# Optimization experiments

Hardware: AMD Instinct MI355X
Metric: run time of the kernel (lower is better)

## Reference

```python
import jax, jax.numpy as jnp
import numpy as np

DEPTH = 17                 # levels of the complete binary tree
N = 2**DEPTH - 1           # 131071 nodes, BFS order: children of n are 2n+1, 2n+2
IN_DIM = 128
HID = 128
OUT = 128


def setup_inputs() -> dict:
    key = jax.random.key(0)
    ks = jax.random.split(key, 20)

    def lin_w(k, o, i):
        s = 1.0 / np.sqrt(i)
        return jax.random.uniform(k, (o, i), minval=-s, maxval=s, dtype=jnp.float32)

    def lin_b(k, o, i):
        s = 1.0 / np.sqrt(i)
        return jax.random.uniform(k, (o,), minval=-s, maxval=s, dtype=jnp.float32)

    inp = {"x": jax.random.normal(ks[0], (N, IN_DIM), dtype=jnp.float32)}
    # complete binary tree, parent -> child edges (row0=src/parent, row1=dst/child)
    child = np.arange(1, N)
    parent = (child - 1) // 2
    inp["edge_index"] = jnp.asarray(np.stack([parent, child]), dtype=jnp.int32)
    names = [("Wi", "bWi", IN_DIM), ("Ui", "bUi", HID),
             ("Wf", "bWf", IN_DIM), ("Uf", "bUf", HID),
             ("Wo", "bWo", IN_DIM), ("Uo", "bUo", HID),
             ("Wu", "bWu", IN_DIM), ("Uu", "bUu", HID)]
    ki = 1
    for wname, bname, idim in names:
        inp[wname] = lin_w(ks[ki], HID, idim)
        inp[bname] = lin_b(ks[ki + 1], HID, idim)
        ki += 2
    inp["Wp"] = lin_w(ks[17], OUT, HID)
    inp["bWp"] = lin_b(ks[18], OUT, HID)
    return inp


def reference(x, edge_index, Wi, bWi, Ui, bUi, Wf, bWf, Uf, bUf,
              Wo, bWo, Uo, bUo, Wu, bWu, Uu, bUu, Wp, bWp):
    # edge_index encodes the complete binary tree in BFS order (children of n
    # are 2n+1 and 2n+2), so the recursion batches exactly by tree level.
    # Precompute input-side gate projections for ALL nodes in 4 GEMMs
    # (equivalent to calling W_*(x[node]) per node in the torch recursion).
    xi = x @ Wi.T + bWi            # (N, H)
    xf = x @ Wf.T + bWf
    xo = x @ Wo.T + bWo
    xu = x @ Wu.T + bWu

    h_next = None  # hidden states of the level below (children)
    c_next = None
    for d in range(DEPTH - 1, -1, -1):   # bottom-up over tree levels
        s = 2**d - 1                     # first node index of level d
        cnt = 2**d                       # nodes at level d
        li, lf, lo, lu = xi[s:s + cnt], xf[s:s + cnt], xo[s:s + cnt], xu[s:s + cnt]
        if h_next is None:               # leaves: no children, h_sum = 0
            i = jax.nn.sigmoid(li)
            o = jax.nn.sigmoid(lo)
            u = jnp.tanh(lu)
            c = i * u
        else:
            # children of node s+k are at positions 2(s+k)+1, 2(s+k)+2: contiguous
            ch_h = h_next.reshape(cnt, 2, HID)
            ch_c = c_next.reshape(cnt, 2, HID)
            h_sum = ch_h.sum(axis=1)     # child-sum
            i = jax.nn.sigmoid(li + h_sum @ Ui.T + bUi)
            o = jax.nn.sigmoid(lo + h_sum @ Uo.T + bUo)
            u = jnp.tanh(lu + h_sum @ Uu.T + bUu)
            # per-child forget gates: sigmoid(W_f x + U_f h_k)
            f = jax.nn.sigmoid(lf[:, None, :] + jnp.einsum('nkh,gh->nkg', ch_h, Uf) + bUf)
            c = i * u + (f * ch_c).sum(axis=1)
        h = o * jnp.tanh(c)
        h_next, c_next = h, c

    h_root = h_next[0]                   # root node index 0
    # dropout is identity in eval mode
    return h_root @ Wp.T + bWp           # (OUT,)
```

## Files before the change

kernel.cpp:

```cpp
#include <hip/hip_runtime.h>
#include <hip/hip_bf16.h>


#define DEPTH 17
#define NTREE ((1 << DEPTH) - 1)
#define DIM 128
#define XSTR 136
#define HSTR 136
#define CSTR 132

typedef __attribute__((ext_vector_type(8))) short short8;
typedef __attribute__((ext_vector_type(4))) float float4v;

__device__ __forceinline__ float sigm(float v) {
    return __fdividef(1.0f, 1.0f + __expf(-v));
}
__device__ __forceinline__ float ftanh(float v) {
    v = fminf(15.0f, fmaxf(-15.0f, v));
    float e = __expf(2.0f * v);
    return __fdividef(e - 1.0f, e + 1.0f);
}

__device__ __forceinline__ unsigned short f2bf(float f) {
    __bf16 h = (__bf16)f;
    unsigned short r;
    __builtin_memcpy(&r, &h, 2);
    return r;
}
__device__ __forceinline__ float bf2f(unsigned short s) {
    union { unsigned u; float f; } a; a.u = ((unsigned)s) << 16;
    return a.f;
}

struct WPtrs {
    const float* W[4];  const float* U[4];
    const float* bW[4]; const float* bU[4];
};

__global__ __launch_bounds__(256) void prep_kernel(WPtrs p, unsigned short* __restrict__ Bsw,
                                                   float* __restrict__ biasWU, float* __restrict__ biasL) {
    int idx = blockIdx.x * 256 + threadIdx.x;
    int j = idx & 7;
    int lane = (idx >> 3) & 63;
    int g = (idx >> 9) & 3;
    int ks = (idx >> 11) & 7;
    int w = idx >> 14;
    int L = lane & 15, q = lane >> 4;
    int c = w * 16 + L;
    int k = ks * 32 + q * 8 + j;
    float v = (k < 128) ? p.W[g][c * 128 + k] * (g == 3 ? 1.0f : 0.5f)
                        : p.U[g][c * 128 + (k - 128)];
    Bsw[idx] = f2bf(v);
    if (idx < 512) {
        int gg = idx >> 7, cc = idx & 127;
        biasWU[idx] = p.bW[gg][cc] + p.bU[gg][cc];
        biasL[idx]  = p.bW[gg][cc];
    }
}

template <bool LEAF0>
__global__ __launch_bounds__(512, 2) void kd2r_kernel(
    const float* __restrict__ x, const unsigned short* __restrict__ Bsw,
    const float* __restrict__ biasL, const float* __restrict__ biasWU,
    unsigned short* __restrict__ hbf, float* __restrict__ cbuf,
    int x0base, int x1base, int ntiles) {
    __shared__ __align__(16) unsigned short xs[2][48 * XSTR];
    __shared__ __align__(16) unsigned short hc[LEAF0 ? 16 : 64 * XSTR];
    __shared__ __align__(16) unsigned short h0[32 * XSTR];
    __shared__ __align__(16) unsigned short c0[32 * XSTR];
    __shared__ __align__(16) unsigned short hA1[16 * XSTR];
    __shared__ __align__(16) float cA1[16 * CSTR];

    const int tid = threadIdx.x;
    const int w = tid >> 6, lane = tid & 63, L = lane & 15, q = lane >> 4;
    const int ch = w * 16 + L;

    short8 b[32];
#pragma unroll
    for (int t = 0; t < 32; ++t)
        b[t] = *(const short8*)(Bsw + ((size_t)w << 14) + (t << 9) + lane * 8);

    float4 pfx[3];
    {
        const long tt = blockIdx.x;
        const long n0 = (long)x0base + tt * 32, n1 = (long)x1base + tt * 16;
#pragma unroll
        for (int k = 0; k < 3; ++k) {
            const int i = tid + 512 * k;
            const int row = i >> 5, j = i & 31;
            const long node = (row < 32) ? (n0 + row) : (n1 + (row - 32));
            pfx[k] = *(const float4*)(x + (size_t)node * DIM + j * 4);
        }
    }

    for (int it = 0; it < ntiles; ++it) {
        const long tt = (long)it * gridDim.x + blockIdx.x;
        const long n0 = (long)x0base + tt * 32;
        const long n1 = (long)x1base + tt * 16;
        const long cb = 2 * n0 + 1;
        const int pc = it & 1;
        unsigned short* xsp = xs[pc];

#pragma unroll
        for (int k = 0; k < 3; ++k) {
            const int i = tid + 512 * k;
            const int row = i >> 5, j = i & 31;
            ushort4 o;
            o.x = f2bf(pfx[k].x); o.y = f2bf(pfx[k].y);
            o.z = f2bf(pfx[k].z); o.w = f2bf(pfx[k].w);
            *(ushort4*)(xsp + row * XSTR + j * 4) = o;
        }
        if (!LEAF0) {
            for (int i = tid; i < 64 * 16; i += 512) {
                const int row = i >> 4, g = i & 15;
                *(uint4*)(hc + row * XSTR + g * 8) =
                    *(const uint4*)(hbf + (size_t)(cb + row) * DIM + g * 8);
            }
        }
        __syncthreads();

        if (it + 1 < ntiles) {
            const long tn = tt + gridDim.x;
            const long m0 = (long)x0base + tn * 32, m1 = (long)x1base + tn * 16;
#pragma unroll
            for (int k = 0; k < 3; ++k) {
                const int i = tid + 512 * k;
                const int row = i >> 5, j = i & 31;
                const long node = (row < 32) ? (m0 + row) : (m1 + (row - 32));
                pfx[k] = *(const float4*)(x + (size_t)node * DIM + j * 4);
            }
        }

        if (it > 0) {
            const long pn1 = n1 - (long)gridDim.x * 16;
            for (int i = tid; i < 16 * 16; i += 512) {
                const int row = i >> 4, g = i & 15;
                *(uint4*)(hbf + (size_t)(pn1 + row) * DIM + g * 8) = *(const uint4*)(hA1 + row * XSTR + g * 8);
            }
            for (int i = tid; i < 16 * 32; i += 512) {
                const int row = i >> 5, j = i & 31;
                *(float4*)(cbuf + (size_t)(pn1 + row) * DIM + j * 4) = *(const float4*)(cA1 + row * CSTR + j * 4);
            }
        }

        if (LEAF0) {
            float4v acc[2][3];
#pragma unroll
            for (int mm = 0; mm < 2; ++mm)
#pragma unroll
                for (int g = 0; g < 3; ++g) acc[mm][g] = (float4v){0.f, 0.f, 0.f, 0.f};
#pragma unroll
            for (int ks = 0; ks < 4; ++ks) {
                short8 a[2];
                a[0] = *(const short8*)(xsp + L * XSTR + ks * 32 + q * 8);
                a[1] = *(const short8*)(xsp + (16 + L) * XSTR + ks * 32 + q * 8);
#pragma unroll
                for (int g = 0; g < 3; ++g)
#pragma unroll
                    for (int mm = 0; mm < 2; ++mm)
                        acc[mm][g] = __builtin_amdgcn_mfma_f32_16x16x32_bf16(a[mm], b[ks * 4 + g], acc[mm][g], 0, 0, 0);
            }
#pragma unroll
            for (int mm = 0; mm < 2; ++mm)
#pragma unroll
                for (int r = 0; r < 4; ++r) {
                    const int nl = 16 * mm + q * 4 + r;
                    float iv = sigm(2.f * acc[mm][0][r] + biasL[ch]);
                    float ov = sigm(2.f * acc[mm][1][r] + biasL[128 + ch]);
                    float uv = ftanh(2.f * acc[mm][2][r] + biasL[256 + ch]);
                    float cv = iv * uv;
                    c0[nl * XSTR + ch] = f2bf(cv);
                    h0[nl * XSTR + ch] = f2bf(ov * ftanh(cv));
                }
        } else {
            for (int mc = 0; mc < 4; mc += 2) {
                float4v acc[2][4];
#pragma unroll
                for (int mm = 0; mm < 2; ++mm)
#pragma unroll
                    for (int g = 0; g < 4; ++g) acc[mm][g] = (float4v){0.f, 0.f, 0.f, 0.f};
#pragma unroll
                for (int ks = 0; ks < 8; ++ks) {
                    const int kk = ks * 32;
                    short8 a[2];
#pragma unroll
                    for (int mm = 0; mm < 2; ++mm) {
                        if (kk < 128)
                            a[mm] = *(const short8*)(xsp + (8 * (mc + mm) + (L >> 1)) * XSTR + kk + q * 8);
                        else
                            a[mm] = *(const short8*)(hc + (16 * (mc + mm) + L) * XSTR + (kk - 128) + q * 8);
                    }
#pragma unroll
                    for (int g = 0; g < 4; ++g)
#pragma unroll
                        for (int mm = 0; mm < 2; ++mm)
                            acc[mm][g] = __builtin_amdgcn_mfma_f32_16x16x32_bf16(a[mm], b[ks * 4 + g], acc[mm][g], 0, 0, 0);
                }
#pragma unroll
                for (int mm = 0; mm < 2; ++mm)
#pragma unroll
                    for (int e = 0; e < 2; ++e) {
                        const int nl = 8 * (mc + mm) + 2 * q + e;
                        const int r0 = 2 * e, r1 = 2 * e + 1;
                        float iv = sigm(acc[mm][0][r0] + acc[mm][0][r1] + biasWU[ch]);
                        float ov = sigm(acc[mm][1][r0] + acc[mm][1][r1] + biasWU[128 + ch]);
                        float uv = ftanh(acc[mm][2][r0] + acc[mm][2][r1] + biasWU[256 + ch]);
                        float fl = sigm(acc[mm][3][r0] + biasWU[384 + ch]);
                        float fr = sigm(acc[mm][3][r1] + biasWU[384 + ch]);
                        float cl = cbuf[(size_t)(cb + 2 * nl) * DIM + ch];
                        float cr = cbuf[(size_t)(cb + 2 * nl + 1) * DIM + ch];
                        float cv = iv * uv + fl * cl + fr * cr;
                        c0[nl * XSTR + ch] = f2bf(cv);
                        h0[nl * XSTR + ch] = f2bf(ov * ftanh(cv));
                    }
            }
        }
        __syncthreads();

        {
            float4v acc[2][4];
#pragma unroll
            for (int mm = 0; mm < 2; ++mm)
#pragma unroll
                for (int g = 0; g < 4; ++g) acc[mm][g] = (float4v){0.f, 0.f, 0.f, 0.f};
#pragma unroll
            for (int ks = 0; ks < 8; ++ks) {
                const int kk = ks * 32;
                short8 a[2];
#pragma unroll
                for (int mm = 0; mm < 2; ++mm) {
                    if (kk < 128)
                        a[mm] = *(const short8*)(xsp + (32 + 8 * mm + (L >> 1)) * XSTR + kk + q * 8);
                    else
                        a[mm] = *(const short8*)(h0 + (16 * mm + L) * XSTR + (kk - 128) + q * 8);
                }
#pragma unroll
                for (int g = 0; g < 4; ++g)
#pragma unroll
                    for (int mm = 0; mm < 2; ++mm)
                        acc[mm][g] = __builtin_amdgcn_mfma_f32_16x16x32_bf16(a[mm], b[ks * 4 + g], acc[mm][g], 0, 0, 0);
            }
#pragma unroll
            for (int mm = 0; mm < 2; ++mm)
#pragma unroll
                for (int e = 0; e < 2; ++e) {
                    const int nl = 8 * mm + 2 * q + e;
                    const int r0 = 2 * e, r1 = 2 * e + 1;
                    float iv = sigm(acc[mm][0][r0] + acc[mm][0][r1] + biasWU[ch]);
                    float ov = sigm(acc[mm][1][r0] + acc[mm][1][r1] + biasWU[128 + ch]);
                    float uv = ftanh(acc[mm][2][r0] + acc[mm][2][r1] + biasWU[256 + ch]);
                    float fl = sigm(acc[mm][3][r0] + biasWU[384 + ch]);
                    float fr = sigm(acc[mm][3][r1] + biasWU[384 + ch]);
                    float cl = bf2f(c0[(2 * nl) * XSTR + ch]);
                    float cr = bf2f(c0[(2 * nl + 1) * XSTR + ch]);
                    float cv = iv * uv + fl * cl + fr * cr;
                    cA1[nl * CSTR + ch] = cv;
                    hA1[nl * XSTR + ch] = f2bf(ov * ftanh(cv));
                }
        }
    }

    __syncthreads();
    {
        const long tl = (long)(ntiles - 1) * gridDim.x + blockIdx.x;
        const long n1 = (long)x1base + tl * 16;
        for (int i = tid; i < 16 * 16; i += 512) {
            const int row = i >> 4, g = i & 15;
            *(uint4*)(hbf + (size_t)(n1 + row) * DIM + g * 8) = *(const uint4*)(hA1 + row * XSTR + g * 8);
        }
        for (int i = tid; i < 16 * 32; i += 512) {
            const int row = i >> 5, j = i & 31;
            *(float4*)(cbuf + (size_t)(n1 + row) * DIM + j * 4) = *(const float4*)(cA1 + row * CSTR + j * 4);
        }
    }
}

template <bool GCH>
__device__ __forceinline__ void internal_level(
    const unsigned short* xc,
    const unsigned short* hin_l, const float* cin_l,
    const unsigned short* __restrict__ hin_g, const float* __restrict__ cin_g, long cb,
    unsigned short* ho, int ho_str, float* co, int co_str, int cnt,
    const short8 (&b)[32], const float* __restrict__ biasWU,
    int L, int q, int ch) {
    const int rows = 2 * cnt;
    const int mt = (rows + 15) >> 4;
    for (int mc = 0; mc < mt; mc += 2) {
        const int mm_n = (mt - mc >= 2) ? 2 : 1;
        float4v acc[2][4];
#pragma unroll
        for (int mm = 0; mm < 2; ++mm)
#pragma unroll
            for (int g = 0; g < 4; ++g) acc[mm][g] = (float4v){0.f, 0.f, 0.f, 0.f};
#pragma unroll
        for (int ks = 0; ks < 8; ++ks) {
            const int kk = ks * 32;
            short8 a[2];
#pragma unroll
            for (int mm = 0; mm < 2; ++mm) {
                if (mm < mm_n) {
                    if (kk < 128) {
                        int xr = 8 * (mc + mm) + (L >> 1);
                        if (xr >= cnt) xr = 0;
                        a[mm] = *(const short8*)(xc + xr * XSTR + kk + q * 8);
                    } else if (!GCH) {
                        a[mm] = *(const short8*)(hin_l + (16 * (mc + mm) + L) * HSTR + (kk - 128) + q * 8);
                    } else {
                        a[mm] = *(const short8*)(hin_g + (size_t)(cb + 16 * (mc + mm) + L) * DIM + (kk - 128) + q * 8);
                    }
                }
            }
#pragma unroll
            for (int g = 0; g < 4; ++g)
#pragma unroll
                for (int mm = 0; mm < 2; ++mm)
                    if (mm < mm_n)
                        acc[mm][g] = __builtin_amdgcn_mfma_f32_16x16x32_bf16(a[mm], b[ks * 4 + g], acc[mm][g], 0, 0, 0);
        }
#pragma unroll
        for (int mm = 0; mm < 2; ++mm)
#pragma unroll
            for (int e = 0; e < 2; ++e) {
                if (mm < mm_n) {
                    const int nl = 8 * (mc + mm) + 2 * q + e;
                    if (nl < cnt) {
                        const int r0 = 2 * e, r1 = 2 * e + 1;
                        float iv = sigm(acc[mm][0][r0] + acc[mm][0][r1] + biasWU[ch]);
                        float ov = sigm(acc[mm][1][r0] + acc[mm][1][r1] + biasWU[128 + ch]);
                        float uv = ftanh(acc[mm][2][r0] + acc[mm][2][r1] + biasWU[256 + ch]);
                        float fl = sigm(acc[mm][3][r0] + biasWU[384 + ch]);
                        float fr = sigm(acc[mm][3][r1] + biasWU[384 + ch]);
                        float cl, cr;
                        if (!GCH) {
                            cl = cin_l[(2 * nl) * CSTR + ch];
                            cr = cin_l[(2 * nl + 1) * CSTR + ch];
                        } else {
                            cl = cin_g[(size_t)(cb + 2 * nl) * DIM + ch];
                            cr = cin_g[(size_t)(cb + 2 * nl + 1) * DIM + ch];
                        }
                        float cv = iv * uv + fl * cl + fr * cr;
                        co[nl * co_str + ch] = cv;
                        ho[nl * ho_str + ch] = f2bf(ov * ftanh(cv));
                    }
                }
            }
    }
}

template <int C, int NL, bool PROJ>
__global__ __launch_bounds__(512, 2) void k23_kernel(
    const float* __restrict__ x, const unsigned short* __restrict__ Bsw,
    const float* __restrict__ biasWU, unsigned short* __restrict__ hbf,
    float* __restrict__ cbuf, int d0,
    const float* __restrict__ Wp, const float* __restrict__ bWp,
    float* __restrict__ out) {
    constexpr int TOTX = 2 * C - (C >> (NL - 1));
    constexpr int AR = (C < 16) ? 16 : C;
    __shared__ __align__(16) unsigned short xs[TOTX * XSTR];
    __shared__ __align__(16) unsigned short hA[AR * HSTR];
    __shared__ __align__(16) unsigned short hB[16 * HSTR];
    __shared__ __align__(16) float cA[AR * CSTR];
    __shared__ __align__(16) float cB[16 * CSTR];
    __shared__ float red[4][128];

    const int tid = threadIdx.x;
    const int w = tid >> 6, lane = tid & 63, L = lane & 15, q = lane >> 4;
    const int ch = w * 16 + L;

    short8 b[32];
#pragma unroll
    for (int t = 0; t < 32; ++t)
        b[t] = *(const short8*)(Bsw + ((size_t)w << 14) + (t << 9) + lane * 8);

    {
        int xoff = 0;
#pragma unroll
        for (int l = 0; l < NL; ++l) {
            const int rows = C >> l;
            const long base = ((1 << (d0 - l)) - 1) + (long)blockIdx.x * rows;
            for (int i = tid; i < rows * 32; i += 512) {
                const int row = i >> 5, j = i & 31;
                float4 v = *(const float4*)(x + (size_t)(base + row) * DIM + j * 4);
                ushort4 o;
                o.x = f2bf(v.x); o.y = f2bf(v.y); o.z = f2bf(v.z); o.w = f2bf(v.w);
                *(ushort4*)(xs + (xoff + row) * XSTR + j * 4) = o;
            }
            xoff += rows;
        }
    }
    __syncthreads();

    const long cb = ((1 << (d0 + 1)) - 1) + (long)blockIdx.x * (2 * C);
    internal_level<true>(xs, nullptr, nullptr, hbf, cbuf, cb,
                         hA, HSTR, cA, CSTR, C, b, biasWU, L, q, ch);
    __syncthreads();

    const unsigned short* hin = hA;
    const float* cin = cA;
    int xoff = C;
#pragma unroll
    for (int l = 1; l < NL; ++l) {
        const int cnt = C >> l;
        if (!PROJ && l == NL - 1) {
            const long ob = ((1 << (d0 - (NL - 1))) - 1) + (long)blockIdx.x;
            internal_level<false>(xs + xoff * XSTR, hin, cin, nullptr, nullptr, 0,
                                  hbf + (size_t)ob * DIM, DIM,
                                  cbuf + (size_t)ob * DIM, DIM, cnt, b, biasWU, L, q, ch);
        } else {
            unsigned short* ho = (l & 1) ? hB : hA;
            float* co = (l & 1) ? cB : cA;
            internal_level<false>(xs + xoff * XSTR, hin, cin, nullptr, nullptr, 0,
                                  ho, HSTR, co, CSTR, cnt, b, biasWU, L, q, ch);
            __syncthreads();
            hin = ho; cin = co;
        }
        xoff += cnt;
    }

    if (PROJ) {
        const int o = tid & 127, sg = tid >> 7;
        float pacc = 0.f;
#pragma unroll
        for (int jj = 0; jj < 8; ++jj) {
            const int k = sg * 32 + jj * 4;
            float4 wv = *(const float4*)(Wp + o * DIM + k);
            pacc += bf2f(hin[k]) * wv.x + bf2f(hin[k + 1]) * wv.y +
                    bf2f(hin[k + 2]) * wv.z + bf2f(hin[k + 3]) * wv.w;
        }
        red[sg][o] = pacc;
        __syncthreads();
        if (tid < 128) out[tid] = bWp[tid] + red[0][tid] + red[1][tid] + red[2][tid] + red[3][tid];
    }
}

extern "C" void kernel_launch(void* const* d_in, const int* in_sizes, int n_in,
                              void* d_out, int out_size, void* d_ws, size_t ws_size,
                              hipStream_t stream) {
    const float* x   = (const float*)d_in[0];
    const float* Wi  = (const float*)d_in[2];  const float* bWi = (const float*)d_in[3];
    const float* Ui  = (const float*)d_in[4];  const float* bUi = (const float*)d_in[5];
    const float* Wf  = (const float*)d_in[6];  const float* bWf = (const float*)d_in[7];
    const float* Uf  = (const float*)d_in[8];  const float* bUf = (const float*)d_in[9];
    const float* Wo  = (const float*)d_in[10]; const float* bWo = (const float*)d_in[11];
    const float* Uo  = (const float*)d_in[12]; const float* bUo = (const float*)d_in[13];
    const float* Wu  = (const float*)d_in[14]; const float* bWu = (const float*)d_in[15];
    const float* Uu  = (const float*)d_in[16]; const float* bUu = (const float*)d_in[17];
    const float* Wp  = (const float*)d_in[18]; const float* bWp = (const float*)d_in[19];

    unsigned short* Bsw = (unsigned short*)d_ws;
    float* biasWU = (float*)(Bsw + 131072);
    float* biasL  = biasWU + 512;
    float* cbuf   = biasL + 512;
    unsigned short* hbf = (unsigned short*)(cbuf + (size_t)65536 * DIM);

    WPtrs p;
    p.W[0] = Wi; p.W[1] = Wo; p.W[2] = Wu; p.W[3] = Wf;
    p.U[0] = Ui; p.U[1] = Uo; p.U[2] = Uu; p.U[3] = Uf;
    p.bW[0] = bWi; p.bW[1] = bWo; p.bW[2] = bWu; p.bW[3] = bWf;
    p.bU[0] = bUi; p.bU[1] = bUo; p.bU[2] = bUu; p.bU[3] = bUf;

    prep_kernel<<<512, 256, 0, stream>>>(p, Bsw, biasWU, biasL);

    kd2r_kernel<true><<<256, 512, 0, stream>>>(x, Bsw, biasL, biasWU, hbf, cbuf,
                                               (1 << 16) - 1, (1 << 15) - 1, 8);
    kd2r_kernel<false><<<256, 512, 0, stream>>>(x, Bsw, biasL, biasWU, hbf, cbuf,
                                                (1 << 14) - 1, (1 << 13) - 1, 2);
    kd2r_kernel<false><<<128, 512, 0, stream>>>(x, Bsw, biasL, biasWU, hbf, cbuf,
                                                (1 << 12) - 1, (1 << 11) - 1, 1);
    k23_kernel<32, 6, false><<<32, 512, 0, stream>>>(x, Bsw, biasWU, hbf, cbuf, 10,
                                                     nullptr, nullptr, nullptr);
    k23_kernel<16, 5, true><<<1, 512, 0, stream>>>(x, Bsw, biasWU, hbf, cbuf, 4,
                                                   Wp, bWp, (float*)d_out);
}
```

Before: 243.3 us.

## Fuse tail kernels into one persistent kernel with grid barriers

Replaces four separate tail launches (two kd2r passes and two k23 passes) with a single 256-block kernel. The stages are separated by atomic-counter grid barriers whose counters are zeroed in the prep kernel. The intent is to remove launch gaps and repeated weight-register loads for the small upper-tree levels. It also drops the tanh clamp and uses the 1-2/(e+1) form. The grid barrier relies on all 256 blocks being co-resident, and most blocks sit idle in the later stages.

```diff
diff --git a/kernel.cpp b/kernel.cpp
--- a/kernel.cpp
+++ b/kernel.cpp
@@ -16,9 +16,8 @@
     return __fdividef(1.0f, 1.0f + __expf(-v));
 }
 __device__ __forceinline__ float ftanh(float v) {
-    v = fminf(15.0f, fmaxf(-15.0f, v));
     float e = __expf(2.0f * v);
-    return __fdividef(e - 1.0f, e + 1.0f);
+    return 1.0f - __fdividef(2.0f, e + 1.0f);
 }
 
 __device__ __forceinline__ unsigned short f2bf(float f) {
@@ -38,7 +37,8 @@
 };
 
 __global__ __launch_bounds__(256) void prep_kernel(WPtrs p, unsigned short* __restrict__ Bsw,
-                                                   float* __restrict__ biasWU, float* __restrict__ biasL) {
+                                                   float* __restrict__ biasWU, float* __restrict__ biasL,
+                                                   unsigned* __restrict__ bar) {
     int idx = blockIdx.x * 256 + threadIdx.x;
     int j = idx & 7;
     int lane = (idx >> 3) & 63;
@@ -56,6 +56,7 @@
         biasWU[idx] = p.bW[gg][cc] + p.bU[gg][cc];
         biasL[idx]  = p.bW[gg][cc];
     }
+    if (idx < 4) bar[idx] = 0u;
 }
 
 template <bool LEAF0>
@@ -272,6 +273,136 @@
             const int row = i >> 5, j = i & 31;
             *(float4*)(cbuf + (size_t)(n1 + row) * DIM + j * 4) = *(const float4*)(cA1 + row * CSTR + j * 4);
         }
+    }
+}
+
+__device__ __forceinline__ void gbar(unsigned* cnt, unsigned target) {
+    __syncthreads();
+    if (threadIdx.x == 0) {
+        __threadfence();
+        atomicAdd(cnt, 1u);
+        while (__hip_atomic_load(cnt, __ATOMIC_RELAXED, __HIP_MEMORY_SCOPE_AGENT) < target)
+            __builtin_amdgcn_s_sleep(2);
+        __threadfence();
+    }
+    __syncthreads();
+}
+
+__device__ void kd2_tile(const float* __restrict__ x, const short8 (&b)[32],
+                         const float* __restrict__ biasWU,
+                         unsigned short* __restrict__ hbf, float* __restrict__ cbuf,
+                         long n0, long n1,
+                         unsigned short* xs, unsigned short* hc, unsigned short* h0,
+                         unsigned short* c0, unsigned short* hA1, float* cA1,
+                         int tid, int L, int q, int ch) {
+    const long cb = 2 * n0 + 1;
+    for (int i = tid; i < 48 * 32; i += 512) {
+        const int row = i >> 5, j = i & 31;
+        const long node = (row < 32) ? (n0 + row) : (n1 + (row - 32));
+        float4 v = *(const float4*)(x + (size_t)node * DIM + j * 4);
+        ushort4 o;
+        o.x = f2bf(v.x); o.y = f2bf(v.y); o.z = f2bf(v.z); o.w = f2bf(v.w);
+        *(ushort4*)(xs + row * XSTR + j * 4) = o;
+    }
+    for (int i = tid; i < 64 * 16; i += 512) {
+        const int row = i >> 4, g = i & 15;
+        *(uint4*)(hc + row * XSTR + g * 8) = *(const uint4*)(hbf + (size_t)(cb + row) * DIM + g * 8);
+    }
+    __syncthreads();
+
+    for (int mc = 0; mc < 4; mc += 2) {
+        float4v acc[2][4];
+#pragma unroll
+        for (int mm = 0; mm < 2; ++mm)
+#pragma unroll
+            for (int g = 0; g < 4; ++g) acc[mm][g] = (float4v){0.f, 0.f, 0.f, 0.f};
+#pragma unroll
+        for (int ks = 0; ks < 8; ++ks) {
+            const int kk = ks * 32;
+            short8 a[2];
+#pragma unroll
+            for (int mm = 0; mm < 2; ++mm) {
+                if (kk < 128)
+                    a[mm] = *(const short8*)(xs + (8 * (mc + mm) + (L >> 1)) * XSTR + kk + q * 8);
+                else
+                    a[mm] = *(const short8*)(hc + (16 * (mc + mm) + L) * XSTR + (kk - 128) + q * 8);
+            }
+#pragma unroll
+            for (int g = 0; g < 4; ++g)
+#pragma unroll
+                for (int mm = 0; mm < 2; ++mm)
+                    acc[mm][g] = __builtin_amdgcn_mfma_f32_16x16x32_bf16(a[mm], b[ks * 4 + g], acc[mm][g], 0, 0, 0);
+        }
+#pragma unroll
+        for (int mm = 0; mm < 2; ++mm)
+#pragma unroll
+            for (int e = 0; e < 2; ++e) {
+                const int nl = 8 * (mc + mm) + 2 * q + e;
+                const int r0 = 2 * e, r1 = 2 * e + 1;
+                float iv = sigm(acc[mm][0][r0] + acc[mm][0][r1] + biasWU[ch]);
+                float ov = sigm(acc[mm][1][r0] + acc[mm][1][r1] + biasWU[128 + ch]);
+                float uv = ftanh(acc[mm][2][r0] + acc[mm][2][r1] + biasWU[256 + ch]);
+                float fl = sigm(acc[mm][3][r0] + biasWU[384 + ch]);
+                float fr = sigm(acc[mm][3][r1] + biasWU[384 + ch]);
+                float cl = cbuf[(size_t)(cb + 2 * nl) * DIM + ch];
+                float cr = cbuf[(size_t)(cb + 2 * nl + 1) * DIM + ch];
+                float cv = iv * uv + fl * cl + fr * cr;
+                c0[nl * XSTR + ch] = f2bf(cv);
+                h0[nl * XSTR + ch] = f2bf(ov * ftanh(cv));
+            }
+    }
+    __syncthreads();
+
+    {
+        float4v acc[2][4];
+#pragma unroll
+        for (int mm = 0; mm < 2; ++mm)
+#pragma unroll
+            for (int g = 0; g < 4; ++g) acc[mm][g] = (float4v){0.f, 0.f, 0.f, 0.f};
+#pragma unroll
+        for (int ks = 0; ks < 8; ++ks) {
+            const int kk = ks * 32;
+            short8 a[2];
+#pragma unroll
+            for (int mm = 0; mm < 2; ++mm) {
+                if (kk < 128)
+                    a[mm] = *(const short8*)(xs + (32 + 8 * mm + (L >> 1)) * XSTR + kk + q * 8);
+                else
+                    a[mm] = *(const short8*)(h0 + (16 * mm + L) * XSTR + (kk - 128) + q * 8);
+            }
+#pragma unroll
+            for (int g = 0; g < 4; ++g)
+#pragma unroll
+                for (int mm = 0; mm < 2; ++mm)
+                    acc[mm][g] = __builtin_amdgcn_mfma_f32_16x16x32_bf16(a[mm], b[ks * 4 + g], acc[mm][g], 0, 0, 0);
+        }
+#pragma unroll
+        for (int mm = 0; mm < 2; ++mm)
+#pragma unroll
+            for (int e = 0; e < 2; ++e) {
+                const int nl = 8 * mm + 2 * q + e;
+                const int r0 = 2 * e, r1 = 2 * e + 1;
+                float iv = sigm(acc[mm][0][r0] + acc[mm][0][r1] + biasWU[ch]);
+                float ov = sigm(acc[mm][1][r0] + acc[mm][1][r1] + biasWU[128 + ch]);
+                float uv = ftanh(acc[mm][2][r0] + acc[mm][2][r1] + biasWU[256 + ch]);
+                float fl = sigm(acc[mm][3][r0] + biasWU[384 + ch]);
+                float fr = sigm(acc[mm][3][r1] + biasWU[384 + ch]);
+                float cl = bf2f(c0[(2 * nl) * XSTR + ch]);
+                float cr = bf2f(c0[(2 * nl + 1) * XSTR + ch]);
+                float cv = iv * uv + fl * cl + fr * cr;
+                cA1[nl * CSTR + ch] = cv;
+                hA1[nl * XSTR + ch] = f2bf(ov * ftanh(cv));
+            }
+    }
+    __syncthreads();
+
+    for (int i = tid; i < 16 * 16; i += 512) {
+        const int row = i >> 4, g = i & 15;
+        *(uint4*)(hbf + (size_t)(n1 + row) * DIM + g * 8) = *(const uint4*)(hA1 + row * XSTR + g * 8);
+    }
+    for (int i = tid; i < 16 * 32; i += 512) {
+        const int row = i >> 5, j = i & 31;
+        *(float4*)(cbuf + (size_t)(n1 + row) * DIM + j * 4) = *(const float4*)(cA1 + row * CSTR + j * 4);
     }
 }
 
@@ -348,36 +479,21 @@
 }
 
 template <int C, int NL, bool PROJ>
-__global__ __launch_bounds__(512, 2) void k23_kernel(
-    const float* __restrict__ x, const unsigned short* __restrict__ Bsw,
-    const float* __restrict__ biasWU, unsigned short* __restrict__ hbf,
-    float* __restrict__ cbuf, int d0,
-    const float* __restrict__ Wp, const float* __restrict__ bWp,
-    float* __restrict__ out) {
-    constexpr int TOTX = 2 * C - (C >> (NL - 1));
-    constexpr int AR = (C < 16) ? 16 : C;
-    __shared__ __align__(16) unsigned short xs[TOTX * XSTR];
-    __shared__ __align__(16) unsigned short hA[AR * HSTR];
-    __shared__ __align__(16) unsigned short hB[16 * HSTR];
-    __shared__ __align__(16) float cA[AR * CSTR];
-    __shared__ __align__(16) float cB[16 * CSTR];
-    __shared__ float red[4][128];
-
-    const int tid = threadIdx.x;
-    const int w = tid >> 6, lane = tid & 63, L = lane & 15, q = lane >> 4;
-    const int ch = w * 16 + L;
-
-    short8 b[32];
-#pragma unroll
-    for (int t = 0; t < 32; ++t)
-        b[t] = *(const short8*)(Bsw + ((size_t)w << 14) + (t << 9) + lane * 8);
-
+__device__ void k23_body(const float* __restrict__ x, const short8 (&b)[32],
+                         const float* __restrict__ biasWU,
+                         unsigned short* __restrict__ hbf, float* __restrict__ cbuf,
+                         int d0, int bx,
+                         unsigned short* xs, unsigned short* hA, unsigned short* hB,
+                         float* cA, float* cB, float* red,
+                         const float* __restrict__ Wp, const float* __restrict__ bWp,
+                         float* __restrict__ out,
+                         int tid, int L, int q, int ch) {
     {
         int xoff = 0;
 #pragma unroll
         for (int l = 0; l < NL; ++l) {
             const int rows = C >> l;
-            const long base = ((1 << (d0 - l)) - 1) + (long)blockIdx.x * rows;
+            const long base = ((1 << (d0 - l)) - 1) + (long)bx * rows;
             for (int i = tid; i < rows * 32; i += 512) {
                 const int row = i >> 5, j = i & 31;
                 float4 v = *(const float4*)(x + (size_t)(base + row) * DIM + j * 4);
@@ -390,7 +506,7 @@
     }
     __syncthreads();
 
-    const long cb = ((1 << (d0 + 1)) - 1) + (long)blockIdx.x * (2 * C);
+    const long cb = ((1 << (d0 + 1)) - 1) + (long)bx * (2 * C);
     internal_level<true>(xs, nullptr, nullptr, hbf, cbuf, cb,
                          hA, HSTR, cA, CSTR, C, b, biasWU, L, q, ch);
     __syncthreads();
@@ -402,7 +518,7 @@
     for (int l = 1; l < NL; ++l) {
         const int cnt = C >> l;
         if (!PROJ && l == NL - 1) {
-            const long ob = ((1 << (d0 - (NL - 1))) - 1) + (long)blockIdx.x;
+            const long ob = ((1 << (d0 - (NL - 1))) - 1) + (long)bx;
             internal_level<false>(xs + xoff * XSTR, hin, cin, nullptr, nullptr, 0,
                                   hbf + (size_t)ob * DIM, DIM,
                                   cbuf + (size_t)ob * DIM, DIM, cnt, b, biasWU, L, q, ch);
@@ -427,10 +543,69 @@
             pacc += bf2f(hin[k]) * wv.x + bf2f(hin[k + 1]) * wv.y +
                     bf2f(hin[k + 2]) * wv.z + bf2f(hin[k + 3]) * wv.w;
         }
-        red[sg][o] = pacc;
+        red[sg * 128 + o] = pacc;
         __syncthreads();
-        if (tid < 128) out[tid] = bWp[tid] + red[0][tid] + red[1][tid] + red[2][tid] + red[3][tid];
-    }
+        if (tid < 128) out[tid] = bWp[tid] + red[tid] + red[128 + tid] + red[256 + tid] + red[384 + tid];
+    }
+}
+
+__global__ __launch_bounds__(512, 2) void tail_kernel(
+    const float* __restrict__ x, const unsigned short* __restrict__ Bsw,
+    const float* __restrict__ biasWU,
+    unsigned short* __restrict__ hbf, float* __restrict__ cbuf,
+    const float* __restrict__ Wp, const float* __restrict__ bWp,
+    float* __restrict__ out, unsigned* __restrict__ bar) {
+    __shared__ __align__(16) unsigned short pool[30336];
+
+    const int tid = threadIdx.x;
+    const int w = tid >> 6, lane = tid & 63, L = lane & 15, q = lane >> 4;
+    const int ch = w * 16 + L;
+
+    short8 b[32];
+#pragma unroll
+    for (int t = 0; t < 32; ++t)
+        b[t] = *(const short8*)(Bsw + ((size_t)w << 14) + (t << 9) + lane * 8);
+
+    unsigned short* xsB  = pool;
+    unsigned short* hcB  = pool + 6528;
+    unsigned short* h0B  = pool + 15232;
+    unsigned short* c0B  = pool + 19584;
+    unsigned short* hA1B = pool + 23936;
+    float*          cA1B = (float*)(pool + 26112);
+
+    for (int it = 0; it < 2; ++it) {
+        const long tt = (long)it * 256 + blockIdx.x;
+        kd2_tile(x, b, biasWU, hbf, cbuf,
+                 (long)((1 << 14) - 1) + tt * 32, (long)((1 << 13) - 1) + tt * 16,
+                 xsB, hcB, h0B, c0B, hA1B, cA1B, tid, L, q, ch);
+    }
+    gbar(bar + 0, 256);
+
+    if (blockIdx.x < 128) {
+        const long tt = blockIdx.x;
+        kd2_tile(x, b, biasWU, hbf, cbuf,
+                 (long)((1 << 12) - 1) + tt * 32, (long)((1 << 11) - 1) + tt * 16,
+                 xsB, hcB, h0B, c0B, hA1B, cA1B, tid, L, q, ch);
+    }
+    gbar(bar + 1, 256);
+
+    unsigned short* xsK = pool;
+    unsigned short* hAK = pool + 8568;
+    unsigned short* hBK = pool + 12920;
+    float*          cAK = (float*)(pool + 15096);
+    float*          cBK = (float*)(pool + 23544);
+    float*          redK = (float*)(pool + 27768);
+
+    if (blockIdx.x < 32)
+        k23_body<32, 6, false>(x, b, biasWU, hbf, cbuf, 10, blockIdx.x,
+                               xsK, hAK, hBK, cAK, cBK, redK,
+                               nullptr, nullptr, nullptr, tid, L, q, ch);
+    gbar(bar + 2, 256);
+
+    if (blockIdx.x == 0)
+        k23_body<16, 5, true>(x, b, biasWU, hbf, cbuf, 4, 0,
+                              xsK, hAK, hBK, cAK, cBK, redK,
+                              Wp, bWp, out, tid, L, q, ch);
 }
 
 extern "C" void kernel_launch(void* const* d_in, const int* in_sizes, int n_in,
@@ -452,6 +627,7 @@
     float* biasL  = biasWU + 512;
     float* cbuf   = biasL + 512;
     unsigned short* hbf = (unsigned short*)(cbuf + (size_t)65536 * DIM);
+    unsigned* bar = (unsigned*)(hbf + (size_t)65536 * DIM);
 
     WPtrs p;
     p.W[0] = Wi; p.W[1] = Wo; p.W[2] = Wu; p.W[3] = Wf;
@@ -459,16 +635,10 @@
     p.bW[0] = bWi; p.bW[1] = bWo; p.bW[2] = bWu; p.bW[3] = bWf;
     p.bU[0] = bUi; p.bU[1] = bUo; p.bU[2] = bUu; p.bU[3] = bUf;
 
-    prep_kernel<<<512, 256, 0, stream>>>(p, Bsw, biasWU, biasL);
+    prep_kernel<<<512, 256, 0, stream>>>(p, Bsw, biasWU, biasL, bar);
 
     kd2r_kernel<true><<<256, 512, 0, stream>>>(x, Bsw, biasL, biasWU, hbf, cbuf,
                                                (1 << 16) - 1, (1 << 15) - 1, 8);
-    kd2r_kernel<false><<<256, 512, 0, stream>>>(x, Bsw, biasL, biasWU, hbf, cbuf,
-                                                (1 << 14) - 1, (1 << 13) - 1, 2);
-    kd2r_kernel<false><<<128, 512, 0, stream>>>(x, Bsw, biasL, biasWU, hbf, cbuf,
-                                                (1 << 12) - 1, (1 << 11) - 1, 1);
-    k23_kernel<32, 6, false><<<32, 512, 0, stream>>>(x, Bsw, biasWU, hbf, cbuf, 10,
-                                                     nullptr, nullptr, nullptr);
-    k23_kernel<16, 5, true><<<1, 512, 0, stream>>>(x, Bsw, biasWU, hbf, cbuf, 4,
-                                                   Wp, bWp, (float*)d_out);
-}
+    tail_kernel<<<256, 512, 0, stream>>>(x, Bsw, biasWU, hbf, cbuf,
+                                         Wp, bWp, (float*)d_out, bar);
+}
```

Measured after the change: 299.0 us. 1.23x slower.
